# Performance work log

Hardware: AMD Instinct MI355X
Metric: run time of the kernel (lower is better)

The kernel has to match this reference:

```python
import jax, jax.numpy as jnp
import numpy as np

N_NODES = 50000
IN_CH = 128
HIDDEN = 64
OUT = 32
HEADS = 4


def _gat_conv(x, src, dst, W, a_src, a_dst, b, heads, ch, concat):
    """PyG-style GATConv (eval mode, self-loops already in src/dst)."""
    N = x.shape[0]
    h = (x @ W).reshape(N, heads, ch)                      # [N,H,C]
    asrc = jnp.einsum('nhc,hc->nh', h, a_src)              # [N,H]
    adst = jnp.einsum('nhc,hc->nh', h, a_dst)              # [N,H]
    e = jax.nn.leaky_relu(asrc[src] + adst[dst], 0.2)      # [E,H]
    # segment softmax over edges grouped by destination node
    m = jax.ops.segment_max(e, dst, num_segments=N)        # [N,H]
    e = jnp.exp(e - m[dst])
    z = jax.ops.segment_sum(e, dst, num_segments=N)        # [N,H]
    alpha = e / (z[dst] + 1e-16)                           # [E,H]
    out = jax.ops.segment_sum(h[src] * alpha[:, :, None], dst, num_segments=N)  # [N,H,C]
    out = out.reshape(N, heads * ch) if concat else out.mean(axis=1)
    return out + b


def _layer_norm(x, g, b):
    mu = x.mean(axis=-1, keepdims=True)
    var = ((x - mu) ** 2).mean(axis=-1, keepdims=True)
    return (x - mu) * jax.lax.rsqrt(var + 1e-5) * g + b


def setup_inputs() -> dict:
    key = jax.random.key(0)
    ks = jax.random.split(key, 20)
    HID = HEADS * HIDDEN  # 256
    s = 0.1
    inp = {
        'x': jax.random.normal(ks[0], (N_NODES, IN_CH), jnp.float32),
        'edge_index': jax.random.randint(ks[1], (2, 800000), 0, N_NODES, jnp.int64 if jax.config.jax_enable_x64 else jnp.int32),
        # conv1
        'W1': jax.random.normal(ks[2], (IN_CH, HID), jnp.float32) * s,
        'a1_src': jax.random.normal(ks[3], (HEADS, HIDDEN), jnp.float32) * s,
        'a1_dst': jax.random.normal(ks[4], (HEADS, HIDDEN), jnp.float32) * s,
        'b1': jnp.zeros((HID,), jnp.float32),
        'g1': jnp.ones((HID,), jnp.float32),
        'be1': jnp.zeros((HID,), jnp.float32),
        # conv2
        'W2': jax.random.normal(ks[5], (HID, HID), jnp.float32) * s,
        'a2_src': jax.random.normal(ks[6], (HEADS, HIDDEN), jnp.float32) * s,
        'a2_dst': jax.random.normal(ks[7], (HEADS, HIDDEN), jnp.float32) * s,
        'b2': jnp.zeros((HID,), jnp.float32),
        'g2': jnp.ones((HID,), jnp.float32),
        'be2': jnp.zeros((HID,), jnp.float32),
        # conv3 (heads=1)
        'W3': jax.random.normal(ks[8], (HID, OUT), jnp.float32) * s,
        'a3_src': jax.random.normal(ks[9], (1, OUT), jnp.float32) * s,
        'a3_dst': jax.random.normal(ks[10], (1, OUT), jnp.float32) * s,
        'b3': jnp.zeros((OUT,), jnp.float32),
    }
    return inp


def reference(x, edge_index, W1, a1_src, a1_dst, b1, g1, be1,
              W2, a2_src, a2_dst, b2, g2, be2,
              W3, a3_src, a3_dst, b3):
    N = x.shape[0]
    loops = jnp.arange(N, dtype=edge_index.dtype)
    ei = jnp.concatenate([edge_index, jnp.stack([loops, loops])], axis=1)
    src, dst = ei[0], ei[1]
    h = _gat_conv(x, src, dst, W1, a1_src, a1_dst, b1, HEADS, HIDDEN, True)
    h = jax.nn.elu(_layer_norm(h, g1, be1))
    h = _gat_conv(h, src, dst, W2, a2_src, a2_dst, b2, HEADS, HIDDEN, True)
    h = jax.nn.elu(_layer_norm(h, g2, be2))
    return _gat_conv(h, src, dst, W3, a3_src, a3_dst, b3, 1, OUT, True)
```

## Files before the change

### kernel.cpp

```cpp
#include <hip/hip_runtime.h>
#include <math.h>

#define NN 50000

typedef __attribute__((ext_vector_type(8))) short bf16x8;
typedef __attribute__((ext_vector_type(4))) float f32x4;

__device__ inline float wred_max(float v){
  #pragma unroll
  for(int s=32;s>0;s>>=1) v=fmaxf(v,__shfl_xor(v,s,64));
  return v;
}
__device__ inline float wred_sum(float v){
  #pragma unroll
  for(int s=32;s>0;s>>=1) v+=__shfl_xor(v,s,64);
  return v;
}
__device__ inline float lrelu(float x){ return x>0.f? x : 0.2f*x; }
__device__ inline float rlf(float v,int l){ return __int_as_float(__builtin_amdgcn_readlane(__float_as_int(v),l)); }

__device__ inline ushort f2bf(float f){
  union{float f;unsigned u;} v; v.f=f;
  unsigned u=v.u;
  return (ushort)((u + 0x7fffu + ((u>>16)&1u)) >> 16);
}
__device__ inline float bflo(unsigned u){ return __uint_as_float(u<<16); }
__device__ inline float bfhi(unsigned u){ return __uint_as_float(u&0xffff0000u); }

__device__ inline void gload_lds16(const void* g, void* l){
  __builtin_amdgcn_global_load_lds((const __attribute__((address_space(1))) void*)g,
                                   (__attribute__((address_space(3))) void*)l, 16, 0, 0);
}

__global__ void casttr3_k(const float* __restrict__ W1,const float* __restrict__ W2,
                          const float* __restrict__ W3,
                          ushort* __restrict__ w1t,ushort* __restrict__ w2t,ushort* __restrict__ w3t){
  int i=blockIdx.x*256+threadIdx.x;
  if(i<32768){ int k=i>>8, n=i&255; w1t[n*128+k]=f2bf(W1[i]); }
  else if(i<98304){ int j=i-32768; int k=j>>8, n=j&255; w2t[n*256+k]=f2bf(W2[j]); }
  else { int j=i-98304; int k=j>>5, n=j&31; w3t[n*256+k]=f2bf(W3[j]); }
}

__global__ void hist_k(const int* __restrict__ dstA,int* __restrict__ counts,int E){
  int i=blockIdx.x*blockDim.x+threadIdx.x;
  if(i<E) atomicAdd(&counts[dstA[i]],1);
}

__global__ __launch_bounds__(1024) void scan1_k(int* __restrict__ counts,int* __restrict__ offs,
                                                int* __restrict__ bsum,int N){
  __shared__ int stot[16];
  int t=threadIdx.x; int lane=t&63, wv=t>>6;
  int base=blockIdx.x*1024;
  int orig=(base+t<N)?counts[base+t]:0;
  int v=orig;
  #pragma unroll
  for(int s=1;s<64;s<<=1){ int u=__shfl_up(v,s,64); if(lane>=s) v+=u; }
  if(lane==63) stot[wv]=v;
  __syncthreads();
  if(wv==0){
    int tv=(lane<16)?stot[lane]:0;
    #pragma unroll
    for(int s=1;s<16;s<<=1){ int u=__shfl_up(tv,s,64); if(lane>=s) tv+=u; }
    if(lane<16) stot[lane]=tv;
  }
  __syncthreads();
  int wpref=(wv>0)?stot[wv-1]:0;
  if(base+t<N){ offs[base+t]=wpref+v-orig; counts[base+t]=0; }
  if(t==1023) bsum[blockIdx.x]=stot[15];
}
__global__ __launch_bounds__(1024) void scan3_k(int* __restrict__ offs,const int* __restrict__ bsum,int N,int E){
  __shared__ int sbase;
  int t=threadIdx.x;
  if(t<64){
    int v=(t<(int)blockIdx.x)?bsum[t]:0;
    #pragma unroll
    for(int s=32;s>0;s>>=1) v+=__shfl_xor(v,s,64);
    if(t==0) sbase=v;
  }
  __syncthreads();
  int i=blockIdx.x*1024+t;
  if(i<N) offs[i]+=sbase;
  if(i==N-1) offs[N]=E;
}

__global__ void scatter_k(const int* __restrict__ srcA,const int* __restrict__ dstA,
                          const int* __restrict__ offs,int* cur,int* __restrict__ ssrc,int E){
  int i=blockIdx.x*blockDim.x+threadIdx.x;
  if(i<E){ int d=dstA[i]; int p=offs[d]+atomicAdd(&cur[d],1); ssrc[p]=srcA[i]; }
}

template<int WR,int WC,int MI,int NI,int DOTM,int AF32>
__global__ __launch_bounds__(256,2) void gemm_bf16_k(const void* __restrict__ Av,
    const ushort* __restrict__ Bt, ushort* __restrict__ C,
    const float* __restrict__ aS, const float* __restrict__ aD,
    float* __restrict__ as_, float* __restrict__ ad_,
    int M, int N, int K){
  constexpr int BM = WR*MI*16;
  constexpr int BN = WC*NI*16;
  __shared__ ushort sA[BM*32];
  __shared__ ushort sB[BN*32];
  int tid=threadIdx.x;
  int lane=tid&63, w=tid>>6;
  int wr=w/WC, wc=w%WC;
  int bm=blockIdx.y*BM, bn=blockIdx.x*BN;
  f32x4 acc[MI][NI]={};

  for(int k0=0;k0<K;k0+=32){
    if constexpr (AF32){
      const float* A=(const float*)Av;
      #pragma unroll
      for(int p=0;p<(BM*4)/256;p++){
        int idx=tid+p*256;
        int r=idx>>2, cs=idx&3;
        int c=cs^(r&3);
        int gr=min(bm+r,M-1);
        float4 v0=*(const float4*)(A+(size_t)gr*K+k0+c*8);
        float4 v1=*(const float4*)(A+(size_t)gr*K+k0+c*8+4);
        ulonglong2 pk;
        pk.x=(unsigned long long)f2bf(v0.x)|((unsigned long long)f2bf(v0.y)<<16)
            |((unsigned long long)f2bf(v0.z)<<32)|((unsigned long long)f2bf(v0.w)<<48);
        pk.y=(unsigned long long)f2bf(v1.x)|((unsigned long long)f2bf(v1.y)<<16)
            |((unsigned long long)f2bf(v1.z)<<32)|((unsigned long long)f2bf(v1.w)<<48);
        *(ulonglong2*)(sA+r*32+cs*8)=pk;
      }
    } else {
      const ushort* A=(const ushort*)Av;
      #pragma unroll
      for(int rr=0;rr<2;rr++){
        int rbase=w*32+rr*16;
        int r=rbase+(lane>>2);
        int cs=lane&3;
        int c=cs^(r&3);
        int gr=min(bm+r,M-1);
        gload_lds16(A+(size_t)gr*K+k0+c*8, sA+rbase*32);
      }
    }
    {
      #pragma unroll
      for(int i=0;i<(BN/16+3)/4;i++){
        int ii=w+i*4;
        if(ii<BN/16){
          int rbase=ii*16;
          int r=rbase+(lane>>2);
          int cs=lane&3;
          int c=cs^(r&3);
          gload_lds16(Bt+(size_t)(bn+r)*K+k0+c*8, sB+rbase*32);
        }
      }
    }
    __syncthreads();
    bf16x8 af[MI], bf[NI];
    #pragma unroll
    for(int m=0;m<MI;m++){
      int rA=(wr*MI+m)*16+(lane&15);
      af[m]=*(bf16x8*)(sA+rA*32+(((lane>>4)^(rA&3))*8));
    }
    #pragma unroll
    for(int n=0;n<NI;n++){
      int rB=(wc*NI+n)*16+(lane&15);
      bf[n]=*(bf16x8*)(sB+rB*32+(((lane>>4)^(rB&3))*8));
    }
    #pragma unroll
    for(int m=0;m<MI;m++)
      #pragma unroll
      for(int n=0;n<NI;n++)
        acc[m][n]=__builtin_amdgcn_mfma_f32_16x16x32_bf16(af[m],bf[n],acc[m][n],0,0,0);
    __syncthreads();
  }
  int rb=lane>>4, cl=lane&15;
  float av[NI], dv[NI];
  #pragma unroll
  for(int n=0;n<NI;n++){
    int gc=bn+(wc*NI+n)*16+cl;
    if constexpr (DOTM!=0){ av[n]=aS[gc]; dv[n]=aD[gc]; }
    else { av[n]=0.f; dv[n]=0.f; }
  }
  #pragma unroll
  for(int m=0;m<MI;m++){
    #pragma unroll
    for(int i=0;i<4;i++){
      int gr=bm+(wr*MI+m)*16+rb*4+i;
      if constexpr (DOTM==1){
        int h=(bn>>6)+wc;
        float ps=0.f,pd=0.f;
        #pragma unroll
        for(int n=0;n<NI;n++){ ps+=acc[m][n][i]*av[n]; pd+=acc[m][n][i]*dv[n]; }
        #pragma unroll
        for(int msk=1;msk<16;msk<<=1){
          ps+=__shfl_xor(ps,msk,64); pd+=__shfl_xor(pd,msk,64);
        }
        if(cl==0 && gr<M){ as_[gr*4+h]=ps; ad_[gr*4+h]=pd; }
      } else if constexpr (DOTM==2){
        float ps=0.f,pd=0.f;
        #pragma unroll
        for(int n=0;n<NI;n++){ ps+=acc[m][n][i]*av[n]; pd+=acc[m][n][i]*dv[n]; }
        #pragma unroll
        for(int msk=1;msk<16;msk<<=1){
          ps+=__shfl_xor(ps,msk,64); pd+=__shfl_xor(pd,msk,64);
        }
        if(cl==0 && gr<M){ as_[gr]=ps; ad_[gr]=pd; }
      }
      if(gr<M){
        #pragma unroll
        for(int n=0;n<NI;n++){
          int gc=bn+(wc*NI+n)*16+cl;
          C[(size_t)gr*N+gc]=f2bf(acc[m][n][i]);
        }
      }
    }
  }
}

__global__ __launch_bounds__(256,6) void agg4_k(const ushort* __restrict__ hb,
    const float* __restrict__ as_,const float* __restrict__ ad_,
    const int* __restrict__ offs,const int* __restrict__ ssrc,
    const float* __restrict__ bias,const float* __restrict__ g,const float* __restrict__ be,
    ushort* __restrict__ outb,int N){
  __shared__ float wlds[4][64][4];
  int lane=threadIdx.x&63, wv=threadIdx.x>>6;
  int n=blockIdx.x*4+wv; if(n>=N) return;
  int lane4=lane*4;
  int h=lane>>4;
  float ad[4], es[4];
  #pragma unroll
  for(int k=0;k<4;k++) ad[k]=ad_[n*4+k];
  #pragma unroll
  for(int k=0;k<4;k++) es[k]=lrelu(as_[n*4+k]+ad[k]);
  int o0=offs[n],o1=offs[n+1];
  int cnt=o1-o0;
  float m[4], inv[4], acc[4];

  if(cnt<=64){
    int sv=0;
    float lv[4]={-1e30f,-1e30f,-1e30f,-1e30f};
    if(lane<cnt){
      sv=ssrc[o0+lane];
      float4 avv=*(const float4*)(as_+(size_t)sv*4);
      lv[0]=lrelu(avv.x+ad[0]); lv[1]=lrelu(avv.y+ad[1]);
      lv[2]=lrelu(avv.z+ad[2]); lv[3]=lrelu(avv.w+ad[3]);
    }
    #pragma unroll
    for(int k=0;k<4;k++) m[k]=fmaxf(es[k],wred_max(lv[k]));
    float w4[4];
    #pragma unroll
    for(int k=0;k<4;k++) w4[k]=(lane<cnt)?__expf(lv[k]-m[k]):0.f;
    #pragma unroll
    for(int k=0;k<4;k++){
      float z=wred_sum(w4[k])+__expf(es[k]-m[k]);
      inv[k]=1.f/(z+1e-16f);
    }
    #pragma unroll
    for(int k=0;k<4;k++) w4[k]*=inv[k];
    *(float4*)&wlds[wv][lane][0]=make_float4(w4[0],w4[1],w4[2],w4[3]);
    asm volatile("s_waitcnt lgkmcnt(0)":::"memory");
    {
      float wself=__expf(es[h]-m[h])*inv[h];
      uint2 u=*(const uint2*)(hb+(size_t)n*256+lane4);
      acc[0]=wself*bflo(u.x); acc[1]=wself*bfhi(u.x);
      acc[2]=wself*bflo(u.y); acc[3]=wself*bfhi(u.y);
    }
    int nbat=(cnt+15)>>4;
    for(int b=0;b<nbat;b++){
      int e0=b*16;
      uint2 u[16];
      #pragma unroll
      for(int i=0;i<16;i++){
        int s=__builtin_amdgcn_readlane(sv,e0+i);
        u[i]=*(const uint2*)(hb+((size_t)s<<8)+lane4);
      }
      #pragma unroll
      for(int i=0;i<16;i++){
        float we=wlds[wv][e0+i][h];
        acc[0]+=we*bflo(u[i].x);
        acc[1]+=we*bfhi(u[i].x);
        acc[2]+=we*bflo(u[i].y);
        acc[3]+=we*bfhi(u[i].y);
      }
    }
  } else {
    #pragma unroll
    for(int k=0;k<4;k++) m[k]=es[k];
    {
      float lm[4]={-1e30f,-1e30f,-1e30f,-1e30f};
      for(int j=o0+lane;j<o1;j+=64){
        int s=ssrc[j];
        float4 avv=*(const float4*)(as_+(size_t)s*4);
        float a[4]={avv.x,avv.y,avv.z,avv.w};
        #pragma unroll
        for(int k=0;k<4;k++) lm[k]=fmaxf(lm[k],lrelu(a[k]+ad[k]));
      }
      #pragma unroll
      for(int k=0;k<4;k++) m[k]=fmaxf(m[k],wred_max(lm[k]));
    }
    {
      float lz[4]={0.f,0.f,0.f,0.f};
      for(int j=o0+lane;j<o1;j+=64){
        int s=ssrc[j];
        float4 avv=*(const float4*)(as_+(size_t)s*4);
        float a[4]={avv.x,avv.y,avv.z,avv.w};
        #pragma unroll
        for(int k=0;k<4;k++) lz[k]+=__expf(lrelu(a[k]+ad[k])-m[k]);
      }
      #pragma unroll
      for(int k=0;k<4;k++){
        float z=wred_sum(lz[k])+__expf(es[k]-m[k]);
        inv[k]=1.f/(z+1e-16f);
      }
    }
    {
      float wself=__expf(es[h]-m[h])*inv[h];
      uint2 u=*(const uint2*)(hb+(size_t)n*256+lane4);
      acc[0]=wself*bflo(u.x); acc[1]=wself*bfhi(u.x);
      acc[2]=wself*bflo(u.y); acc[3]=wself*bfhi(u.y);
    }
    for(int base=o0;base<o1;base+=64){
      int c2=min(64,o1-base);
      int j=base+lane;
      int sv=0; float w4[4]={0.f,0.f,0.f,0.f};
      if(j<o1){
        sv=ssrc[j];
        float4 avv=*(const float4*)(as_+(size_t)sv*4);
        float a[4]={avv.x,avv.y,avv.z,avv.w};
        #pragma unroll
        for(int k=0;k<4;k++) w4[k]=__expf(lrelu(a[k]+ad[k])-m[k])*inv[k];
      }
      for(int t=0;t<c2;t++){
        int s=__builtin_amdgcn_readlane(sv,t);
        float wa=rlf(w4[0],t),wb=rlf(w4[1],t),wc=rlf(w4[2],t),wd=rlf(w4[3],t);
        float we = h<2 ? (h==0?wa:wb) : (h==2?wc:wd);
        uint2 u=*(const uint2*)(hb+(size_t)s*256+lane4);
        acc[0]+=we*bflo(u.x);
        acc[1]+=we*bfhi(u.x);
        acc[2]+=we*bflo(u.y);
        acc[3]+=we*bfhi(u.y);
      }
    }
  }
  {
    float4 bv=*(const float4*)(bias+lane4);
    acc[0]+=bv.x; acc[1]+=bv.y; acc[2]+=bv.z; acc[3]+=bv.w;
  }
  float tot=wred_sum(acc[0]+acc[1]+acc[2]+acc[3]);
  float mu=tot*(1.f/256.f);
  float vs=0.f;
  #pragma unroll
  for(int k=0;k<4;k++){ float d=acc[k]-mu; vs+=d*d; }
  float var=wred_sum(vs)*(1.f/256.f);
  float r=rsqrtf(var+1e-5f);
  float4 gv=*(const float4*)(g+lane4);
  float4 bev=*(const float4*)(be+lane4);
  float gg[4]={gv.x,gv.y,gv.z,gv.w};
  float bb[4]={bev.x,bev.y,bev.z,bev.w};
  unsigned long long pk=0;
  #pragma unroll
  for(int k=0;k<4;k++){
    float v=(acc[k]-mu)*r*gg[k]+bb[k];
    float ev= v>0.f? v : expm1f(v);
    pk|=((unsigned long long)f2bf(ev))<<(16*k);
  }
  *(unsigned long long*)(outb+(size_t)n*256+lane4)=pk;
}

__global__ __launch_bounds__(256) void agg1_k(const ushort* __restrict__ hb,
    const float* __restrict__ as_,const float* __restrict__ ad_,
    const int* __restrict__ offs,const int* __restrict__ ssrc,
    const float* __restrict__ bias,float* __restrict__ out,int N){
  int lane=threadIdx.x&63, wv=threadIdx.x>>6;
  int n=blockIdx.x*4+wv; if(n>=N) return;
  float ad=ad_[n];
  float es=lrelu(as_[n]+ad);
  int o0=offs[n],o1=offs[n+1];
  int cnt=o1-o0;
  float m, inv, acc=0.f;
  int lane32=lane&31;
  int half=lane>>5;

  if(cnt<=64){
    int sv=0; float lv=-1e30f;
    if(lane<cnt){ sv=ssrc[o0+lane]; lv=lrelu(as_[sv]+ad); }
    m=fmaxf(es,wred_max(lv));
    float w1=(lane<cnt)?__expf(lv-m):0.f;
    float z=wred_sum(w1)+__expf(es-m);
    inv=1.f/(z+1e-16f);
    w1*=inv;
    if(half==0) acc=__expf(es-m)*inv*__uint_as_float(((unsigned)hb[(size_t)n*32+lane32])<<16);
    int cnt2=(cnt+1)&~1;
    for(int t=0;t<cnt2;t+=2){
      int sL=__builtin_amdgcn_readlane(sv,t);
      int sH=__builtin_amdgcn_readlane(sv,t+1);
      float wL=rlf(w1,t), wH=rlf(w1,t+1);
      int s = half? sH : sL;
      float ww = half? wH : wL;
      float hv=__uint_as_float(((unsigned)hb[(size_t)s*32+lane32])<<16);
      acc+=ww*hv;
    }
    acc+=__shfl_xor(acc,32,64);
  } else {
    m=es;
    {
      float lm=-1e30f;
      for(int j=o0+lane;j<o1;j+=64) lm=fmaxf(lm,lrelu(as_[ssrc[j]]+ad));
      m=fmaxf(m,wred_max(lm));
    }
    {
      float lz=0.f;
      for(int j=o0+lane;j<o1;j+=64) lz+=__expf(lrelu(as_[ssrc[j]]+ad)-m);
      float z=wred_sum(lz)+__expf(es-m);
      inv=1.f/(z+1e-16f);
    }
    if(lane<32) acc=__expf(es-m)*inv*__uint_as_float(((unsigned)hb[(size_t)n*32+lane])<<16);
    for(int base=o0;base<o1;base+=64){
      int c2=min(64,o1-base);
      int j=base+lane;
      int sv=0; float w1=0.f;
      if(j<o1){ sv=ssrc[j]; w1=__expf(lrelu(as_[sv]+ad)-m)*inv; }
      for(int t=0;t<c2;t++){
        int s=__builtin_amdgcn_readlane(sv,t);
        if(lane<32) acc+=rlf(w1,t)*__uint_as_float(((unsigned)hb[(size_t)s*32+lane])<<16);
      }
    }
  }
  if(lane<32) out[(size_t)n*32+lane]=acc+bias[lane];
}

extern "C" void kernel_launch(void* const* d_in,const int* in_sizes,int n_in,
                              void* d_out,int out_size,void* d_ws,size_t ws_size,
                              hipStream_t stream){
  const float* x  =(const float*)d_in[0];
  const int*   ei =(const int*)  d_in[1];
  const float* W1 =(const float*)d_in[2];
  const float* a1s=(const float*)d_in[3];
  const float* a1d=(const float*)d_in[4];
  const float* b1 =(const float*)d_in[5];
  const float* g1 =(const float*)d_in[6];
  const float* be1=(const float*)d_in[7];
  const float* W2 =(const float*)d_in[8];
  const float* a2s=(const float*)d_in[9];
  const float* a2d=(const float*)d_in[10];
  const float* b2 =(const float*)d_in[11];
  const float* g2 =(const float*)d_in[12];
  const float* be2=(const float*)d_in[13];
  const float* W3 =(const float*)d_in[14];
  const float* a3s=(const float*)d_in[15];
  const float* a3d=(const float*)d_in[16];
  const float* b3 =(const float*)d_in[17];
  float* outp=(float*)d_out;
  int N=NN;
  int E=in_sizes[1]/2;
  const int* srcA=ei;
  const int* dstA=ei+E;

  char* w=(char*)d_ws;
  ushort* hb =(ushort*)w; w+=(size_t)N*256*2;
  ushort* h3b=(ushort*)w; w+=(size_t)N*32*2;
  ushort* obb=(ushort*)w; w+=(size_t)N*256*2;
  ushort* w1t=(ushort*)w; w+=(size_t)256*128*2;
  ushort* w2t=(ushort*)w; w+=(size_t)256*256*2;
  ushort* w3t=(ushort*)w; w+=(size_t)32*256*2;
  float* asb =(float*)w; w+=(size_t)N*4*4;
  float* adb =(float*)w; w+=(size_t)N*4*4;
  int* offs=(int*)w; w+=(size_t)(N+4)*4;
  int* cur =(int*)w; w+=(size_t)N*4;
  int* ssrc=(int*)w; w+=(size_t)E*4;
  int* bsum=(int*)w; w+=(size_t)64*4;

  int NB=(N+1023)/1024;

  hipMemsetAsync(cur,0,(size_t)N*4,stream);
  hist_k<<<(E+255)/256,256,0,stream>>>(dstA,cur,E);
  scan1_k<<<NB,1024,0,stream>>>(cur,offs,bsum,N);
  scan3_k<<<NB,1024,0,stream>>>(offs,bsum,N,E);
  scatter_k<<<(E+255)/256,256,0,stream>>>(srcA,dstA,offs,cur,ssrc,E);

  casttr3_k<<<416,256,0,stream>>>(W1,W2,W3,w1t,w2t,w3t);

  int nblkN=(N+3)/4;
  int gY128=(N+127)/128;

  gemm_bf16_k<2,2,4,4,1,1><<<dim3(2,gY128),256,0,stream>>>(x,w1t,hb,a1s,a1d,asb,adb,N,256,128);
  agg4_k<<<nblkN,256,0,stream>>>(hb,asb,adb,offs,ssrc,b1,g1,be1,obb,N);

  gemm_bf16_k<2,2,4,4,1,0><<<dim3(2,gY128),256,0,stream>>>(obb,w2t,hb,a2s,a2d,asb,adb,N,256,256);
  agg4_k<<<nblkN,256,0,stream>>>(hb,asb,adb,offs,ssrc,b2,g2,be2,obb,N);

  gemm_bf16_k<4,1,2,2,2,0><<<dim3(1,gY128),256,0,stream>>>(obb,w3t,h3b,a3s,a3d,asb,adb,N,32,256);
  agg1_k<<<nblkN,256,0,stream>>>(h3b,asb,adb,offs,ssrc,b3,outp,N);
}
```

Baseline: 327.4 us.

## Fuse CSR build into a single persistent kernel with grid-wide barriers

Five CSR-construction launches (memset, histogram, two scan kernels, scatter) are replaced by one persistent 49×1024 kernel. It steps through the zeroing, histogram, block scan, offset fix-up and scatter phases, separated by atomic-counter grid barriers. The aim is to remove launch and inter-kernel gap overhead. The trade-off is that the histogram and scatter now run on far fewer threads, and correctness depends on all blocks being co-resident. Separately, the aggregation kernel drops its min-blocks-per-CU launch bound, and the GEMM loader loop is generalised to BM/64 with no change for the current tile sizes.

```diff
diff --git a/kernel.cpp b/kernel.cpp
--- a/kernel.cpp
+++ b/kernel.cpp
@@ -41,52 +41,61 @@
   else { int j=i-98304; int k=j>>5, n=j&31; w3t[n*256+k]=f2bf(W3[j]); }
 }
 
-__global__ void hist_k(const int* __restrict__ dstA,int* __restrict__ counts,int E){
-  int i=blockIdx.x*blockDim.x+threadIdx.x;
-  if(i<E) atomicAdd(&counts[dstA[i]],1);
-}
-
-__global__ __launch_bounds__(1024) void scan1_k(int* __restrict__ counts,int* __restrict__ offs,
-                                                int* __restrict__ bsum,int N){
-  __shared__ int stot[16];
-  int t=threadIdx.x; int lane=t&63, wv=t>>6;
-  int base=blockIdx.x*1024;
-  int orig=(base+t<N)?counts[base+t]:0;
-  int v=orig;
-  #pragma unroll
-  for(int s=1;s<64;s<<=1){ int u=__shfl_up(v,s,64); if(lane>=s) v+=u; }
-  if(lane==63) stot[wv]=v;
+__device__ inline void gsync(int* c,int target){
   __syncthreads();
-  if(wv==0){
-    int tv=(lane<16)?stot[lane]:0;
-    #pragma unroll
-    for(int s=1;s<16;s<<=1){ int u=__shfl_up(tv,s,64); if(lane>=s) tv+=u; }
-    if(lane<16) stot[lane]=tv;
+  if(threadIdx.x==0){
+    __hip_atomic_fetch_add(c,1,__ATOMIC_ACQ_REL,__HIP_MEMORY_SCOPE_AGENT);
+    while(__hip_atomic_load(c,__ATOMIC_ACQUIRE,__HIP_MEMORY_SCOPE_AGENT)<target)
+      __builtin_amdgcn_s_sleep(8);
   }
   __syncthreads();
-  int wpref=(wv>0)?stot[wv-1]:0;
-  if(base+t<N){ offs[base+t]=wpref+v-orig; counts[base+t]=0; }
-  if(t==1023) bsum[blockIdx.x]=stot[15];
-}
-__global__ __launch_bounds__(1024) void scan3_k(int* __restrict__ offs,const int* __restrict__ bsum,int N,int E){
-  __shared__ int sbase;
-  int t=threadIdx.x;
-  if(t<64){
-    int v=(t<(int)blockIdx.x)?bsum[t]:0;
-    #pragma unroll
-    for(int s=32;s>0;s>>=1) v+=__shfl_xor(v,s,64);
-    if(t==0) sbase=v;
-  }
-  __syncthreads();
-  int i=blockIdx.x*1024+t;
-  if(i<N) offs[i]+=sbase;
-  if(i==N-1) offs[N]=E;
-}
-
-__global__ void scatter_k(const int* __restrict__ srcA,const int* __restrict__ dstA,
-                          const int* __restrict__ offs,int* cur,int* __restrict__ ssrc,int E){
-  int i=blockIdx.x*blockDim.x+threadIdx.x;
-  if(i<E){ int d=dstA[i]; int p=offs[d]+atomicAdd(&cur[d],1); ssrc[p]=srcA[i]; }
+}
+
+__global__ __launch_bounds__(1024) void csr_k(const int* __restrict__ srcA,const int* __restrict__ dstA,
+    int* __restrict__ cur,int* __restrict__ offs,int* __restrict__ bsum,int* __restrict__ ssrc,
+    int* sync,int N,int E){
+  int t=threadIdx.x, bid=blockIdx.x;
+  int NBLK=gridDim.x;
+  int gtid=bid*1024+t, gsz=NBLK*1024;
+  for(int i=gtid;i<N;i+=gsz) cur[i]=0;
+  gsync(&sync[0],NBLK);
+  for(int i=gtid;i<E;i+=gsz) atomicAdd(&cur[dstA[i]],1);
+  gsync(&sync[1],NBLK);
+  {
+    __shared__ int stot[16];
+    int lane=t&63, wv=t>>6;
+    int idx=bid*1024+t;
+    int orig=(idx<N)?cur[idx]:0;
+    int v=orig;
+    #pragma unroll
+    for(int s=1;s<64;s<<=1){ int u=__shfl_up(v,s,64); if(lane>=s) v+=u; }
+    if(lane==63) stot[wv]=v;
+    __syncthreads();
+    if(wv==0){
+      int tv=(lane<16)?stot[lane]:0;
+      #pragma unroll
+      for(int s=1;s<16;s<<=1){ int u=__shfl_up(tv,s,64); if(lane>=s) tv+=u; }
+      if(lane<16) stot[lane]=tv;
+    }
+    __syncthreads();
+    int wpref=(wv>0)?stot[wv-1]:0;
+    if(idx<N){ offs[idx]=wpref+v-orig; cur[idx]=0; }
+    if(t==1023) bsum[bid]=stot[15];
+  }
+  gsync(&sync[2],NBLK);
+  {
+    int myb=0;
+    for(int j=0;j<bid;j++) myb+=bsum[j];
+    int idx=bid*1024+t;
+    if(idx<N) offs[idx]+=myb;
+    if(bid==0&&t==0) offs[N]=E;
+  }
+  gsync(&sync[3],NBLK);
+  for(int i=gtid;i<E;i+=gsz){
+    int d=dstA[i];
+    int p=offs[d]+atomicAdd(&cur[d],1);
+    ssrc[p]=srcA[i];
+  }
 }
 
 template<int WR,int WC,int MI,int NI,int DOTM,int AF32>
@@ -126,8 +135,8 @@
     } else {
       const ushort* A=(const ushort*)Av;
       #pragma unroll
-      for(int rr=0;rr<2;rr++){
-        int rbase=w*32+rr*16;
+      for(int rr=0;rr<BM/64;rr++){
+        int rbase=w*(BM/4)+rr*16;
         int r=rbase+(lane>>2);
         int cs=lane&3;
         int c=cs^(r&3);
@@ -211,7 +220,7 @@
   }
 }
 
-__global__ __launch_bounds__(256,6) void agg4_k(const ushort* __restrict__ hb,
+__global__ __launch_bounds__(256) void agg4_k(const ushort* __restrict__ hb,
     const float* __restrict__ as_,const float* __restrict__ ad_,
     const int* __restrict__ offs,const int* __restrict__ ssrc,
     const float* __restrict__ bias,const float* __restrict__ g,const float* __restrict__ be,
@@ -463,14 +472,10 @@
   int* cur =(int*)w; w+=(size_t)N*4;
   int* ssrc=(int*)w; w+=(size_t)E*4;
   int* bsum=(int*)w; w+=(size_t)64*4;
-
-  int NB=(N+1023)/1024;
-
-  hipMemsetAsync(cur,0,(size_t)N*4,stream);
-  hist_k<<<(E+255)/256,256,0,stream>>>(dstA,cur,E);
-  scan1_k<<<NB,1024,0,stream>>>(cur,offs,bsum,N);
-  scan3_k<<<NB,1024,0,stream>>>(offs,bsum,N,E);
-  scatter_k<<<(E+255)/256,256,0,stream>>>(srcA,dstA,offs,cur,ssrc,E);
+  int* sync=(int*)w; w+=(size_t)16*4;
+
+  hipMemsetAsync(sync,0,16*4,stream);
+  csr_k<<<49,1024,0,stream>>>(srcA,dstA,cur,offs,bsum,ssrc,sync,N,E);
 
   casttr3_k<<<416,256,0,stream>>>(W1,W2,W3,w1t,w2t,w3t);
 
```

Result: slower. 380.4 us (+16.2%).
